# Kernel optimization log

Measured on AMD Instinct MI355X. Metric: run time of the kernel, lower is better.

Reference implementation:

```python
import jax, jax.numpy as jnp
import numpy as np

C = 256          # in_channels == representation_size (GNN(in_channels, in_channels))
REP = 256
H = 300
W = 300
K = 5            # conv/patch kernel
S = 5            # patch stride
KNN = 7          # node_connectivities[0]
HEADS = 8
NH, NW = H // S, W // S
N = NH * NW      # 3600 graph nodes


def setup_inputs() -> dict:
    key = jax.random.key(0)
    ctr = [0]
    def nk():
        ctr[0] += 1
        return jax.random.fold_in(key, ctr[0])
    def rn(shape, s):
        return jax.random.normal(nk(), shape, dtype=jnp.float32) * s
    d = {}
    d['x'] = jax.random.normal(nk(), (1, C, H, W), dtype=jnp.float32)
    d['conv1_w'] = rn((C, C, K, K), 0.02)
    d['conv1_b'] = jnp.zeros((C,), jnp.float32)
    d['fc2_w'] = rn((C, REP), 0.02)
    d['fc2_b'] = jnp.zeros((REP,), jnp.float32)
    d['fc3_w'] = rn((2 * REP, REP), 0.02)
    d['fc3_b'] = jnp.zeros((REP,), jnp.float32)
    def gat(pfx, fin, heads):
        d[pfx + '_wl'] = rn((fin, heads * REP), 0.03)
        d[pfx + '_bl'] = jnp.zeros((heads * REP,), jnp.float32)
        d[pfx + '_wr'] = rn((fin, heads * REP), 0.03)
        d[pfx + '_br'] = jnp.zeros((heads * REP,), jnp.float32)
        d[pfx + '_att'] = rn((heads, REP), 0.1)
        d[pfx + '_bias'] = jnp.zeros((heads * REP,), jnp.float32)
    gat('g1', REP, HEADS)
    gat('g2', HEADS * REP, 1)
    gat('g3', REP, HEADS)
    gat('g4', HEADS * REP, 1)
    return d


def _gatv2(x, wl, bl, wr, br, att, bias, src, dst, mask):
    # PyG GATv2Conv (eval mode, add_self_loops handled by caller via src/dst/mask)
    heads, F = att.shape
    n = x.shape[0]
    xl = (x @ wl + bl).reshape(n, heads, F)   # source transform
    xr = (x @ wr + br).reshape(n, heads, F)   # target transform
    e = jax.nn.leaky_relu(xl[src] + xr[dst], 0.2)          # [E,H,F]
    logit = jnp.einsum('ehf,hf->eh', e, att)               # [E,H]
    logit = jnp.where(mask[:, None], logit, -1e30)
    m = jax.ops.segment_max(logit, dst, num_segments=n)    # every node has a self loop
    ex = jnp.exp(logit - m[dst]) * mask[:, None]
    denom = jax.ops.segment_sum(ex, dst, num_segments=n)
    alpha = ex / denom[dst]
    out = jax.ops.segment_sum(alpha[:, :, None] * xl[src], dst, num_segments=n)
    return out.reshape(n, heads * F) + bias


def _edges_from_topk(vals, idx, strict):
    # torch: A.scatter(1, idx, vals); triu; nonzero -> (row<=col, val!=0);
    # GATv2Conv then removes self loops and adds one per node.
    rows = jnp.arange(N)
    if strict:
        keep = (rows[:, None] < idx) & (vals != 0)
    else:
        keep = (rows[:, None] <= idx) & (vals != 0)  # diag excluded by vals==0 (cdist self-dist)
    src = jnp.concatenate([idx.ravel(), rows])       # source = column index
    dst = jnp.concatenate([jnp.repeat(rows, KNN), rows])  # target = row index
    mask = jnp.concatenate([keep.ravel(), jnp.ones((N,), bool)])
    return src, dst, mask


def _forward(x, conv1_w, conv1_b, fc2_w, fc2_b, fc3_w, fc3_b,
             g1_wl, g1_bl, g1_wr, g1_br, g1_att, g1_bias,
             g2_wl, g2_bl, g2_wr, g2_br, g2_att, g2_bias,
             g3_wl, g3_bl, g3_wr, g3_br, g3_att, g3_bias,
             g4_wl, g4_bl, g4_wr, g4_br, g4_att, g4_bias):
    # --- non-overlapping 5x5 patch embed: unfold + conv(5)->1x1 output ---
    patches = x[0].reshape(C, NH, K, NW, K).transpose(1, 3, 0, 2, 4).reshape(N, C, K, K)
    emb = jax.nn.relu(jnp.einsum('nckl,ockl->no', patches, conv1_w) + conv1_b)
    emb = jax.nn.relu(emb @ fc2_w + fc2_b)  # [N, REP]  (fc1 is unused in the original forward)

    # --- feature-similarity graph: emb @ emb.T, row-wise top-k, triu ---
    adj = emb @ emb.T
    vals, idx = jax.lax.top_k(adj, KNN)
    src1, dst1, m1 = _edges_from_topk(vals, idx, strict=True)

    # --- spatial kNN graph over region centers (cdist, smallest-k, triu) ---
    yy, xx = jnp.meshgrid(jnp.arange(0, H, S, dtype=jnp.float32),
                          jnp.arange(0, W, S, dtype=jnp.float32), indexing='ij')
    centers = jnp.stack([yy.ravel(), xx.ravel()], -1)    # [N,2], i-major like patches
    sq = jnp.sum(centers * centers, -1)
    dist = jnp.sqrt(jnp.maximum(sq[:, None] + sq[None, :] - 2.0 * (centers @ centers.T), 0.0))
    nv, nidx = jax.lax.top_k(-dist, KNN)
    src2, dst2, m2 = _edges_from_topk(-nv, nidx, strict=False)

    h = jax.nn.elu(_gatv2(emb, g1_wl, g1_bl, g1_wr, g1_br, g1_att, g1_bias, src1, dst1, m1))
    h = jax.nn.elu(_gatv2(h, g2_wl, g2_bl, g2_wr, g2_br, g2_att, g2_bias, src1, dst1, m1))
    h_ = jax.nn.elu(_gatv2(emb, g3_wl, g3_bl, g3_wr, g3_br, g3_att, g3_bias, src2, dst2, m2))
    h_ = jax.nn.elu(_gatv2(h_, g4_wl, g4_bl, g4_wr, g4_br, g4_att, g4_bias, src2, dst2, m2))

    hc = jax.nn.relu(jnp.concatenate([h, h_], axis=1) @ fc3_w + fc3_b)
    return hc + h_


def reference(x, conv1_w, conv1_b, fc2_w, fc2_b, fc3_w, fc3_b,
              g1_wl, g1_bl, g1_wr, g1_br, g1_att, g1_bias,
              g2_wl, g2_bl, g2_wr, g2_br, g2_att, g2_bias,
              g3_wl, g3_bl, g3_wr, g3_br, g3_att, g3_bias,
              g4_wl, g4_bl, g4_wr, g4_br, g4_att, g4_bias):
    return _forward(x, conv1_w, conv1_b, fc2_w, fc2_b, fc3_w, fc3_b,
                    g1_wl, g1_bl, g1_wr, g1_br, g1_att, g1_bias,
                    g2_wl, g2_bl, g2_wr, g2_br, g2_att, g2_bias,
                    g3_wl, g3_bl, g3_wr, g3_br, g3_att, g3_bias,
                    g4_wl, g4_bl, g4_wr, g4_br, g4_att, g4_bias)
```

## Files before the change

### kernel.cpp

```cpp
#include <hip/hip_runtime.h>
#include <hip/hip_bf16.h>
#include <math.h>

#define NN 3600
#define HIMG 300
#define WIMG 300
#define NHP 60
#define NCT 57

typedef __attribute__((ext_vector_type(8))) short bf16x8;
typedef __attribute__((ext_vector_type(4))) float f32x4;

__device__ __forceinline__ float bf2f(unsigned short u) {
  union { unsigned int i; float f; } v; v.i = ((unsigned int)u) << 16; return v.f;
}
__device__ __forceinline__ float ldE(const void* p, long i, int md) {
  return md ? bf2f(((const unsigned short*)p)[i]) : ((const float*)p)[i];
}
__device__ __forceinline__ unsigned short f2bf(float f) {
  __hip_bfloat16 h = __float2bfloat16(f);
  return *(unsigned short*)&h;
}

__global__ __launch_bounds__(256) void detect_mode(
    const unsigned short* __restrict__ x, int* __restrict__ flag) {
  __shared__ int bad;
  if (threadIdx.x == 0) bad = 0;
  __syncthreads();
  int b = 0;
  for (int i = threadIdx.x; i < 8192; i += 256) {
    int e = (x[i] >> 7) & 0xFF;
    if (e >= 0x90) b = 1;
  }
  if (b) atomicOr(&bad, 1);
  __syncthreads();
  if (threadIdx.x == 0) {
    flag[0] = bad ? 0 : 1;
    flag[1] = 0;
  }
}

__global__ __launch_bounds__(256) void wtrans(
    const void* __restrict__ w, float* __restrict__ wT, const int* __restrict__ mode) {
  const int md = *mode;
  __shared__ float t[32][33];
  const int k0 = blockIdx.x * 32, o0 = blockIdx.y * 32;
  const int tx = threadIdx.x & 31, ty = threadIdx.x >> 5;
#pragma unroll
  for (int s = 0; s < 32; s += 8)
    t[ty + s][tx] = ldE(w, (long)(o0 + ty + s) * 6400 + k0 + tx, md);
  __syncthreads();
#pragma unroll
  for (int s = 0; s < 32; s += 8)
    wT[(size_t)(k0 + ty + s) * 256 + o0 + tx] = t[tx][ty + s];
}

__global__ __launch_bounds__(256) void wconvT(
    const void* __restrict__ src, unsigned short* __restrict__ dst,
    int Kd, int Nd, const int* __restrict__ mode) {
  const int md = *mode;
  __shared__ float t[32][33];
  const int k0 = blockIdx.x * 32, n0 = blockIdx.y * 32;
  const int tx = threadIdx.x & 31, ty = threadIdx.x >> 5;
#pragma unroll
  for (int s = 0; s < 32; s += 8)
    t[ty + s][tx] = ldE(src, (long)(k0 + ty + s) * Nd + n0 + tx, md);
  __syncthreads();
#pragma unroll
  for (int s = 0; s < 32; s += 8)
    dst[(size_t)(n0 + ty + s) * Kd + k0 + tx] = f2bf(t[tx][ty + s]);
}

__global__ __launch_bounds__(256) void cvt_bf16(
    const float* __restrict__ src, unsigned short* __restrict__ dst, long n4) {
  for (long i = (long)blockIdx.x * 256 + threadIdx.x; i < n4; i += (long)gridDim.x * 256) {
    float4 v = *(const float4*)(src + i * 4);
    ushort4 o;
    o.x = f2bf(v.x); o.y = f2bf(v.y); o.z = f2bf(v.z); o.w = f2bf(v.w);
    *(ushort4*)(dst + i * 4) = o;
  }
}

__global__ __launch_bounds__(256) void im2col(
    const void* __restrict__ x, float* __restrict__ a2, int h, const int* __restrict__ mode) {
  const int md = *mode;
  const int total = NN * 3200;
  for (int i = blockIdx.x * 256 + threadIdx.x; i < total; i += gridDim.x * 256) {
    int n = i / 3200, kl = i - n * 3200;
    int k = h * 3200 + kl;
    int c = k / 25, q = k - c * 25;
    int ki = q / 5, li = q - ki * 5;
    int ni = n / NHP, nj = n - ni * NHP;
    a2[i] = ldE(x, (long)c * (HIMG * WIMG) + (5 * ni + ki) * WIMG + 5 * nj + li, md);
  }
}

__global__ __launch_bounds__(256) void gemm_f84(
    const float* __restrict__ A, const float* __restrict__ B, long boff,
    float* __restrict__ part, int M, int lda, int kchunk, int ldb) {
  __shared__ float As[16][136];
  __shared__ float Bs[16][68];
  const int m0 = blockIdx.y * 128, n0 = blockIdx.x * 64;
  const int z = blockIdx.z;
  const int tid = threadIdx.x;
  const int tr = tid >> 4, tc = tid & 15;
  const int ar = tid >> 1, akq = tid & 1;
  const int bkr = tid >> 4, bnc = tid & 15;
  const int arow = m0 + ar;
  float acc[8][4] = {};

  const int kb = z * kchunk, ke = kb + kchunk;
  for (int k0 = kb; k0 < ke; k0 += 16) {
    __syncthreads();
    {
      float4 v0 = make_float4(0.f, 0.f, 0.f, 0.f), v1 = v0;
      if (arow < M) {
        const float* ap = A + (size_t)arow * lda + k0 + akq * 8;
        v0 = *(const float4*)ap;
        v1 = *(const float4*)(ap + 4);
      }
      As[akq * 8 + 0][ar] = v0.x;
      As[akq * 8 + 1][ar] = v0.y;
      As[akq * 8 + 2][ar] = v0.z;
      As[akq * 8 + 3][ar] = v0.w;
      As[akq * 8 + 4][ar] = v1.x;
      As[akq * 8 + 5][ar] = v1.y;
      As[akq * 8 + 6][ar] = v1.z;
      As[akq * 8 + 7][ar] = v1.w;
    }
    {
      float4 v = *(const float4*)(B + (size_t)(k0 + bkr) * ldb + boff + n0 + bnc * 4);
      Bs[bkr][bnc * 4 + 0] = v.x;
      Bs[bkr][bnc * 4 + 1] = v.y;
      Bs[bkr][bnc * 4 + 2] = v.z;
      Bs[bkr][bnc * 4 + 3] = v.w;
    }
    __syncthreads();
#pragma unroll
    for (int kk = 0; kk < 16; ++kk) {
      float4 a0 = *(const float4*)&As[kk][tr * 8];
      float4 a1 = *(const float4*)&As[kk][tr * 8 + 4];
      float4 bv = *(const float4*)&Bs[kk][tc * 4];
      float a[8] = {a0.x, a0.y, a0.z, a0.w, a1.x, a1.y, a1.z, a1.w};
      float b[4] = {bv.x, bv.y, bv.z, bv.w};
#pragma unroll
      for (int i = 0; i < 8; ++i)
#pragma unroll
        for (int j = 0; j < 4; ++j) acc[i][j] = fmaf(a[i], b[j], acc[i][j]);
    }
  }
#pragma unroll
  for (int i = 0; i < 8; ++i) {
    int row = m0 + tr * 8 + i;
    if (row < M) {
#pragma unroll
      for (int j = 0; j < 4; ++j)
        part[((size_t)z * M + row) * 256 + n0 + tc * 4 + j] = acc[i][j];
    }
  }
}

template <int STORE, int ACT>
__global__ __launch_bounds__(256) void gemm_u(
    const float* __restrict__ A, const void* __restrict__ B0, const void* __restrict__ B1,
    long boff, const void* __restrict__ bias0, const void* __restrict__ bias1, long biasoff,
    float* __restrict__ C0, float* __restrict__ C1, float* __restrict__ part, int cld,
    int M, int lda, int kchunk, int KS, int ldb, const int* __restrict__ mode) {
  const int md = *mode;
  const int z = blockIdx.z;
  const int pair = z / KS, ks = z - pair * KS;
  const void* B = pair ? B1 : B0;
  const void* bias = pair ? bias1 : bias0;
  float* C = pair ? C1 : C0;
  __shared__ float As[16][68];
  __shared__ float Bs[16][68];
  const int m0 = blockIdx.y * 64, n0 = blockIdx.x * 64;
  const int tid = threadIdx.x;
  const int tr = tid >> 4, tc = tid & 15;
  const int ar = tid >> 2, akq = tid & 3;
  const int bkr = tid >> 4, bnc = tid & 15;
  const int arow = m0 + ar;
  float acc[4][4] = {};

  const int kb = ks * kchunk, ke = kb + kchunk;
  for (int k0 = kb; k0 < ke; k0 += 16) {
    __syncthreads();
    {
      float4 v = make_float4(0.f, 0.f, 0.f, 0.f);
      if (arow < M) v = *(const float4*)(A + (size_t)arow * lda + k0 + akq * 4);
      As[akq * 4 + 0][ar] = v.x;
      As[akq * 4 + 1][ar] = v.y;
      As[akq * 4 + 2][ar] = v.z;
      As[akq * 4 + 3][ar] = v.w;
    }
    {
      long bidx = (long)(k0 + bkr) * ldb + boff + n0 + bnc * 4;
      if (md) {
        ushort4 u = *(const ushort4*)((const unsigned short*)B + bidx);
        Bs[bkr][bnc * 4 + 0] = bf2f(u.x);
        Bs[bkr][bnc * 4 + 1] = bf2f(u.y);
        Bs[bkr][bnc * 4 + 2] = bf2f(u.z);
        Bs[bkr][bnc * 4 + 3] = bf2f(u.w);
      } else {
        float4 v = *(const float4*)((const float*)B + bidx);
        Bs[bkr][bnc * 4 + 0] = v.x;
        Bs[bkr][bnc * 4 + 1] = v.y;
        Bs[bkr][bnc * 4 + 2] = v.z;
        Bs[bkr][bnc * 4 + 3] = v.w;
      }
    }
    __syncthreads();
#pragma unroll
    for (int kk = 0; kk < 16; ++kk) {
      float4 av = *(const float4*)&As[kk][tr * 4];
      float4 bv = *(const float4*)&Bs[kk][tc * 4];
      float a[4] = {av.x, av.y, av.z, av.w};
      float b[4] = {bv.x, bv.y, bv.z, bv.w};
#pragma unroll
      for (int i = 0; i < 4; ++i)
#pragma unroll
        for (int j = 0; j < 4; ++j) acc[i][j] = fmaf(a[i], b[j], acc[i][j]);
    }
  }
#pragma unroll
  for (int i = 0; i < 4; ++i) {
    int row = m0 + tr * 4 + i;
    if (row < M) {
#pragma unroll
      for (int j = 0; j < 4; ++j) {
        int col = n0 + tc * 4 + j;
        if (STORE == 2) {
          part[((size_t)z * M + row) * cld + col] = acc[i][j];
        } else if (STORE == 1) {
          C[(size_t)row * cld + col] += acc[i][j];
        } else {
          float v = acc[i][j] + ldE(bias, biasoff + col, md);
          if (ACT == 1) v = fmaxf(v, 0.f);
          C[(size_t)row * cld + col] = v;
        }
      }
    }
  }
}

template <int STORE>
__global__ __launch_bounds__(256) void gemm_mf(
    const unsigned short* __restrict__ A,
    const unsigned short* __restrict__ B0, const unsigned short* __restrict__ B1,
    const void* __restrict__ bias0, const void* __restrict__ bias1,
    float* __restrict__ C0, float* __restrict__ C1, float* __restrict__ part, int cld,
    int M, int K, int kchunk, int KS, const int* __restrict__ mode) {
  const int md = *mode;
  const int z = blockIdx.z;
  const int pair = z / KS, ks = z - pair * KS;
  const unsigned short* B = pair ? B1 : B0;
  const void* bias = pair ? bias1 : bias0;
  float* C = pair ? C1 : C0;

  __shared__ __align__(16) unsigned short Al[128][40];
  __shared__ __align__(16) unsigned short Bl[128][40];
  const int m0 = blockIdx.y * 128, n0 = blockIdx.x * 128;
  const int tid = threadIdx.x;
  const int lane = tid & 63, w = tid >> 6;
  const int wr = (w >> 1) * 64, wc = (w & 1) * 64;
  const int frow = lane & 15, fk = (lane >> 4) * 8;

  f32x4 acc[4][4];
#pragma unroll
  for (int i = 0; i < 4; ++i)
#pragma unroll
    for (int j = 0; j < 4; ++j) acc[i][j] = (f32x4){0.f, 0.f, 0.f, 0.f};

  const int kb0 = ks * kchunk, ke = kb0 + kchunk;
  for (int kb = kb0; kb < ke; kb += 32) {
    __syncthreads();
    for (int c = tid; c < 512; c += 256) {
      int row = c >> 2, kc = (c & 3) << 3;
      uint4 v = make_uint4(0, 0, 0, 0);
      int gr = m0 + row;
      if (gr < M) v = *(const uint4*)(A + (size_t)gr * K + kb + kc);
      *(uint4*)&Al[row][kc] = v;
    }
    for (int c = tid; c < 512; c += 256) {
      int col = c >> 2, kc = (c & 3) << 3;
      uint4 v = *(const uint4*)(B + (size_t)(n0 + col) * K + kb + kc);
      *(uint4*)&Bl[col][kc] = v;
    }
    __syncthreads();

    bf16x8 af[4], bfr[4];
#pragma unroll
    for (int rt = 0; rt < 4; ++rt)
      af[rt] = *(const bf16x8*)&Al[wr + rt * 16 + frow][fk];
#pragma unroll
    for (int ct = 0; ct < 4; ++ct)
      bfr[ct] = *(const bf16x8*)&Bl[wc + ct * 16 + frow][fk];
#pragma unroll
    for (int rt = 0; rt < 4; ++rt)
#pragma unroll
      for (int ct = 0; ct < 4; ++ct)
        acc[rt][ct] = __builtin_amdgcn_mfma_f32_16x16x32_bf16(af[rt], bfr[ct], acc[rt][ct], 0, 0, 0);
  }

#pragma unroll
  for (int rt = 0; rt < 4; ++rt) {
#pragma unroll
    for (int ct = 0; ct < 4; ++ct) {
      int col = n0 + wc + ct * 16 + (lane & 15);
#pragma unroll
      for (int reg = 0; reg < 4; ++reg) {
        int row = m0 + wr + rt * 16 + ((lane >> 4) << 2) + reg;
        if (row < M) {
          float v = acc[rt][ct][reg];
          if (STORE == 2) {
            part[((size_t)z * M + row) * cld + col] = v;
          } else {
            C[(size_t)row * cld + col] = v + ldE(bias, col, md);
          }
        }
      }
    }
  }
}

template <int ACT, int ADDIN, int BIAS>
__global__ __launch_bounds__(256) void reduce_u(
    const float* __restrict__ part, int KS, int M, int ncols,
    const void* __restrict__ bias0, const void* __restrict__ bias1, long biasoff,
    float* __restrict__ C0, float* __restrict__ C1, int cld, const int* __restrict__ mode) {
  const int md = *mode;
  const int pair = blockIdx.z;
  const void* bias = pair ? bias1 : bias0;
  float* C = pair ? C1 : C0;
  size_t total = (size_t)M * ncols;
  for (size_t i = (size_t)blockIdx.x * blockDim.x + threadIdx.x; i < total;
       i += (size_t)gridDim.x * blockDim.x) {
    int row = (int)(i / ncols), col = (int)(i - (size_t)row * ncols);
    float s = ADDIN ? C[(size_t)row * cld + col] : 0.f;
    for (int ks = 0; ks < KS; ++ks)
      s += part[(((size_t)(pair * KS + ks)) * M + row) * ncols + col];
    if (BIAS) s += ldE(bias, biasoff + col, md);
    if (ACT == 1) s = fmaxf(s, 0.f);
    C[(size_t)row * cld + col] = s;
  }
}

__global__ __launch_bounds__(256) void patch_part(
    const void* __restrict__ x, const void* __restrict__ w,
    float* __restrict__ part, int CPB, const int* __restrict__ mode) {
  const int md = *mode;
  __shared__ float As[25][68];
  __shared__ float Bs[25][68];
  const int m0 = blockIdx.y * 64, n0 = blockIdx.x * 64;
  const int tid = threadIdx.x;
  const int tr = tid >> 4, tc = tid & 15;
  const int z = blockIdx.z;
  float acc[4][4] = {};
  const int c0 = z * CPB;
  for (int c = c0; c < c0 + CPB; ++c) {
    __syncthreads();
    for (int e = tid; e < 1600; e += 256) {
      int p = e / 25, q = e - p * 25;
      int ki = q / 5, li = q - ki * 5;
      int n = m0 + p;
      float v = 0.f;
      if (n < NN) {
        int ni = n / NHP, nj = n - ni * NHP;
        v = ldE(x, (long)c * (HIMG * WIMG) + (5 * ni + ki) * WIMG + 5 * nj + li, md);
      }
      As[q][p] = v;
    }
    for (int e = tid; e < 1600; e += 256) {
      int o = e / 25, q = e - o * 25;
      Bs[q][o] = ldE(w, (long)(n0 + o) * 6400 + c * 25 + q, md);
    }
    __syncthreads();
#pragma unroll
    for (int kk = 0; kk < 25; ++kk) {
      float4 av = *(const float4*)&As[kk][tr * 4];
      float4 bv = *(const float4*)&Bs[kk][tc * 4];
      float a[4] = {av.x, av.y, av.z, av.w};
      float b[4] = {bv.x, bv.y, bv.z, bv.w};
#pragma unroll
      for (int i = 0; i < 4; ++i)
#pragma unroll
        for (int j = 0; j < 4; ++j) acc[i][j] = fmaf(a[i], b[j], acc[i][j]);
    }
  }
#pragma unroll
  for (int i = 0; i < 4; ++i) {
    int row = m0 + tr * 4 + i;
    if (row < NN) {
#pragma unroll
      for (int j = 0; j < 4; ++j)
        part[((size_t)z * NN + row) * 256 + n0 + tc * 4 + j] = acc[i][j];
    }
  }
}

__global__ __launch_bounds__(256) void adj_gemm(
    const float* __restrict__ emb, float* __restrict__ pv, unsigned char* __restrict__ pi) {
  __shared__ float As[16][68];
  __shared__ float Bs[16][68];
  __shared__ float mv[64][68];
  __shared__ unsigned char mi[64][68];
  const int m0 = blockIdx.y * 64, n0 = blockIdx.x * 64;
  const int ct = blockIdx.x;
  const int tid = threadIdx.x;
  const int tr = tid >> 4, tc = tid & 15;
  const int ar = tid >> 2, akq = tid & 3;
  const int bn = tid >> 2, bkq = tid & 3;
  const int arow = m0 + ar;
  const int bcol = n0 + bn;
  float acc[4][4] = {};

  for (int k0 = 0; k0 < 256; k0 += 16) {
    __syncthreads();
    {
      float4 v = make_float4(0.f, 0.f, 0.f, 0.f);
      if (arow < NN) v = *(const float4*)(emb + (size_t)arow * 256 + k0 + akq * 4);
      As[akq * 4 + 0][ar] = v.x;
      As[akq * 4 + 1][ar] = v.y;
      As[akq * 4 + 2][ar] = v.z;
      As[akq * 4 + 3][ar] = v.w;
    }
    {
      float4 v = make_float4(0.f, 0.f, 0.f, 0.f);
      if (bcol < NN) v = *(const float4*)(emb + (size_t)bcol * 256 + k0 + bkq * 4);
      Bs[bkq * 4 + 0][bn] = v.x;
      Bs[bkq * 4 + 1][bn] = v.y;
      Bs[bkq * 4 + 2][bn] = v.z;
      Bs[bkq * 4 + 3][bn] = v.w;
    }
    __syncthreads();
#pragma unroll
    for (int kk = 0; kk < 16; ++kk) {
      float4 av = *(const float4*)&As[kk][tr * 4];
      float4 bv = *(const float4*)&Bs[kk][tc * 4];
      float a[4] = {av.x, av.y, av.z, av.w};
      float b[4] = {bv.x, bv.y, bv.z, bv.w};
#pragma unroll
      for (int i = 0; i < 4; ++i)
#pragma unroll
        for (int j = 0; j < 4; ++j) acc[i][j] = fmaf(a[i], b[j], acc[i][j]);
    }
  }

#pragma unroll
  for (int i = 0; i < 4; ++i) {
    float v[4]; int id[4];
#pragma unroll
    for (int j = 0; j < 4; ++j) {
      int cl = tc * 4 + j;
      int valid = (n0 + cl) < NN;
      v[j] = valid ? acc[i][j] : -1e38f;
      id[j] = valid ? cl : 255;
    }
#pragma unroll
    for (int a = 1; a < 4; ++a) {
      float va = v[a]; int ia = id[a];
      int b = a;
      while (b > 0 && (va > v[b - 1] || (va == v[b - 1] && ia < id[b - 1]))) {
        v[b] = v[b - 1]; id[b] = id[b - 1]; --b;
      }
      v[b] = va; id[b] = ia;
    }
    int rl = tr * 4 + i;
#pragma unroll
    for (int s = 0; s < 4; ++s) {
      mv[rl][tc * 4 + s] = v[s];
      mi[rl][tc * 4 + s] = (unsigned char)id[s];
    }
  }
  __syncthreads();

  if (tid < 64) {
    int row = m0 + tid;
    if (row < NN) {
      int ptr[16];
#pragma unroll
      for (int g = 0; g < 16; ++g) ptr[g] = 0;
      for (int k = 0; k < 7; ++k) {
        float best = -1e38f; int bid = 0x7fffffff; int bg = 0;
        for (int g = 0; g < 16; ++g) {
          if (ptr[g] < 4) {
            float vv = mv[tid][g * 4 + ptr[g]];
            int ii = mi[tid][g * 4 + ptr[g]];
            if (vv > best || (vv == best && ii < bid)) { best = vv; bid = ii; bg = g; }
          }
        }
        ptr[bg]++;
        pv[(size_t)row * (NCT * 7) + ct * 7 + k] = best;
        pi[(size_t)row * (NCT * 7) + ct * 7 + k] = (unsigned char)bid;
      }
    }
  }
}

__global__ __launch_bounds__(256) void adj_merge57(
    const float* __restrict__ pv, const unsigned char* __restrict__ pi,
    int* __restrict__ idx_o, int* __restrict__ keep_o) {
  __shared__ unsigned char sp[256][NCT + 3];
  const int t = threadIdx.x;
  const int row = blockIdx.x * 256 + t;
  for (int c = 0; c < NCT; ++c) sp[t][c] = 0;
  if (row >= NN) return;
  const size_t base = (size_t)row * (NCT * 7);
  for (int k = 0; k < 7; ++k) {
    float best = -1e38f; int bidx = 0x7fffffff; int bct = 0;
    for (int c = 0; c < NCT; ++c) {
      int p = sp[t][c];
      if (p < 7) {
        float v = pv[base + c * 7 + p];
        int ii = c * 64 + (int)pi[base + c * 7 + p];
        if (v > best || (v == best && ii < bidx)) { best = v; bidx = ii; bct = c; }
      }
    }
    sp[t][bct]++;
    idx_o[row * 7 + k] = bidx;
    keep_o[row * 7 + k] = (bidx > row && best != 0.0f) ? 1 : 0;
  }
}

__global__ __launch_bounds__(256) void spatial_topk(int* __restrict__ idx_o, int* __restrict__ keep_o) {
  int r = blockIdx.x * 256 + threadIdx.x;
  if (r >= NN) return;
  int ri = r / NHP, rj = r - (r / NHP) * NHP;
  int bd[7], bi[7];
#pragma unroll
  for (int k = 0; k < 7; ++k) { bd[k] = 0x7fffffff; bi[k] = 0x7fffffff; }
  int ilo = ri - 2 > 0 ? ri - 2 : 0, ihi = ri + 2 < NHP - 1 ? ri + 2 : NHP - 1;
  int jlo = rj - 2 > 0 ? rj - 2 : 0, jhi = rj + 2 < NHP - 1 ? rj + 2 : NHP - 1;
  for (int i2 = ilo; i2 <= ihi; ++i2) {
    int dy = ri - i2; int dy2 = dy * dy;
    for (int j2 = jlo; j2 <= jhi; ++j2) {
      int dx = rj - j2;
      int d = dy2 + dx * dx;
      int m = i2 * NHP + j2;
      if (d < bd[6]) {
        int pq = 6;
        while (pq > 0 && d < bd[pq - 1]) { bd[pq] = bd[pq - 1]; bi[pq] = bi[pq - 1]; --pq; }
        bd[pq] = d; bi[pq] = m;
      }
    }
  }
#pragma unroll
  for (int k = 0; k < 7; ++k) {
    idx_o[r * 7 + k] = bi[k];
    keep_o[r * 7 + k] = (bi[k] >= r && bd[k] != 0) ? 1 : 0;
  }
}

__global__ __launch_bounds__(256) void gat_agg1(
    const float* __restrict__ xl, const float* __restrict__ xr,
    const void* __restrict__ att, long attoff, const void* __restrict__ gbias, long gboff,
    const int* __restrict__ nbr, const int* __restrict__ keep,
    float* __restrict__ out, const int* __restrict__ mode) {
  const int md = *mode;
  const int r = blockIdx.x;
  const int f = threadIdx.x;
  __shared__ int s_src[8];
  __shared__ int s_mask_s;
  __shared__ float red[4][8];
  if (f < 7) {
    int v = nbr[r * 7 + f];
    s_src[f] = ((unsigned)v < (unsigned)NN) ? v : 0;
  }
  if (f == 7) s_src[7] = r;
  if (f == 0) {
    int mk = 0x80;
    for (int e = 0; e < 7; ++e)
      if (keep[r * 7 + e] != 0) mk |= (1 << e);
    s_mask_s = mk;
  }
  __syncthreads();
  const int mask = s_mask_s;
  const int wid = f >> 6, lane = f & 63;

  float xrv = xr[(size_t)r * 256 + f];
  float attv = ldE(att, attoff + f, md);
  float xlv[8], part[8];
#pragma unroll
  for (int e = 0; e < 8; ++e) {
    xlv[e] = 0.f; part[e] = 0.f;
    if (mask & (1 << e)) {
      float v = xl[(size_t)s_src[e] * 256 + f];
      xlv[e] = v;
      float s = v + xrv;
      s = s > 0.f ? s : 0.2f * s;
      part[e] = s * attv;
    }
  }
#pragma unroll
  for (int e = 0; e < 8; ++e) {
    float v = part[e];
#pragma unroll
    for (int off = 32; off > 0; off >>= 1) v += __shfl_xor(v, off, 64);
    if (lane == 0) red[wid][e] = v;
  }
  __syncthreads();
  float m = -1e38f;
  float logit[8];
#pragma unroll
  for (int e = 0; e < 8; ++e) {
    logit[e] = red[0][e] + red[1][e] + red[2][e] + red[3][e];
    if (mask & (1 << e)) m = fmaxf(m, logit[e]);
  }
  float den = 0.f, al[8];
#pragma unroll
  for (int e = 0; e < 8; ++e) {
    al[e] = (mask & (1 << e)) ? expf(logit[e] - m) : 0.f;
    den += al[e];
  }
  float inv = 1.0f / den;
  float o = 0.f;
#pragma unroll
  for (int e = 0; e < 8; ++e) o = fmaf(al[e], xlv[e], o);
  o = o * inv + ldE(gbias, gboff + f, md);
  o = o > 0.f ? o : expm1f(o);
  out[(size_t)r * 256 + f] = o;
}

__global__ __launch_bounds__(256) void gat_agg8h(
    const float* __restrict__ xl, const float* __restrict__ xr,
    const void* __restrict__ att, const void* __restrict__ gbias,
    const int* __restrict__ nbr, const int* __restrict__ keep,
    float* __restrict__ out, const int* __restrict__ mode) {
  const int md = *mode;
  const int r = blockIdx.x;
  const int h = blockIdx.y;
  const int f = threadIdx.x;
  __shared__ int s_src[8];
  __shared__ int s_mask_s;
  __shared__ float red[4][8];
  if (f < 7) {
    int v = nbr[r * 7 + f];
    s_src[f] = ((unsigned)v < (unsigned)NN) ? v : 0;
  }
  if (f == 7) s_src[7] = r;
  if (f == 0) {
    int mk = 0x80;
    for (int e = 0; e < 7; ++e)
      if (keep[r * 7 + e] != 0) mk |= (1 << e);
    s_mask_s = mk;
  }
  __syncthreads();
  const int mask = s_mask_s;
  const int wid = f >> 6, lane = f & 63;

  float xrv = xr[(size_t)r * 2048 + h * 256 + f];
  float attv = ldE(att, h * 256 + f, md);
  float xlv[8], part[8];
#pragma unroll
  for (int e = 0; e < 8; ++e) {
    xlv[e] = 0.f; part[e] = 0.f;
    if (mask & (1 << e)) {
      float v = xl[(size_t)s_src[e] * 2048 + h * 256 + f];
      xlv[e] = v;
      float s = v + xrv;
      s = s > 0.f ? s : 0.2f * s;
      part[e] = s * attv;
    }
  }
#pragma unroll
  for (int e = 0; e < 8; ++e) {
    float v = part[e];
#pragma unroll
    for (int off = 32; off > 0; off >>= 1) v += __shfl_xor(v, off, 64);
    if (lane == 0) red[wid][e] = v;
  }
  __syncthreads();
  float m = -1e38f;
  float logit[8];
#pragma unroll
  for (int e = 0; e < 8; ++e) {
    logit[e] = red[0][e] + red[1][e] + red[2][e] + red[3][e];
    if (mask & (1 << e)) m = fmaxf(m, logit[e]);
  }
  float den = 0.f, al[8];
#pragma unroll
  for (int e = 0; e < 8; ++e) {
    al[e] = (mask & (1 << e)) ? expf(logit[e] - m) : 0.f;
    den += al[e];
  }
  float inv = 1.0f / den;
  float o = 0.f;
#pragma unroll
  for (int e = 0; e < 8; ++e) o = fmaf(al[e], xlv[e], o);
  o = o * inv + ldE(gbias, h * 256 + f, md);
  o = o > 0.f ? o : expm1f(o);
  out[(size_t)r * 2048 + h * 256 + f] = o;
}

__global__ __launch_bounds__(256) void fc3_final(
    const float* __restrict__ h2, const float* __restrict__ h4,
    const void* __restrict__ B, const void* __restrict__ bias,
    void* __restrict__ outp, const int* __restrict__ mode) {
  const int md = *mode;
  __shared__ float As[16][68];
  __shared__ float Bs[16][68];
  const int m0 = blockIdx.y * 64, n0 = blockIdx.x * 64;
  const int tid = threadIdx.x;
  const int tr = tid >> 4, tc = tid & 15;
  const int ar = tid >> 2, akq = tid & 3;
  const int bkr = tid >> 4, bnc = tid & 15;
  const int arow = m0 + ar;
  float acc[4][4] = {};

  for (int k0 = 0; k0 < 512; k0 += 16) {
    __syncthreads();
    {
      int k = k0 + akq * 4;
      float4 v = make_float4(0.f, 0.f, 0.f, 0.f);
      if (arow < NN) {
        const float* src = (k < 256) ? (h2 + (size_t)arow * 256 + k)
                                     : (h4 + (size_t)arow * 256 + (k - 256));
        v = *(const float4*)src;
      }
      As[akq * 4 + 0][ar] = v.x;
      As[akq * 4 + 1][ar] = v.y;
      As[akq * 4 + 2][ar] = v.z;
      As[akq * 4 + 3][ar] = v.w;
    }
    {
      long bidx = (long)(k0 + bkr) * 256 + n0 + bnc * 4;
      if (md) {
        ushort4 u = *(const ushort4*)((const unsigned short*)B + bidx);
        Bs[bkr][bnc * 4 + 0] = bf2f(u.x);
        Bs[bkr][bnc * 4 + 1] = bf2f(u.y);
        Bs[bkr][bnc * 4 + 2] = bf2f(u.z);
        Bs[bkr][bnc * 4 + 3] = bf2f(u.w);
      } else {
        float4 v = *(const float4*)((const float*)B + bidx);
        Bs[bkr][bnc * 4 + 0] = v.x;
        Bs[bkr][bnc * 4 + 1] = v.y;
        Bs[bkr][bnc * 4 + 2] = v.z;
        Bs[bkr][bnc * 4 + 3] = v.w;
      }
    }
    __syncthreads();
#pragma unroll
    for (int kk = 0; kk < 16; ++kk) {
      float4 av = *(const float4*)&As[kk][tr * 4];
      float4 bv = *(const float4*)&Bs[kk][tc * 4];
      float a[4] = {av.x, av.y, av.z, av.w};
      float b[4] = {bv.x, bv.y, bv.z, bv.w};
#pragma unroll
      for (int i = 0; i < 4; ++i)
#pragma unroll
        for (int j = 0; j < 4; ++j) acc[i][j] = fmaf(a[i], b[j], acc[i][j]);
    }
  }
#pragma unroll
  for (int i = 0; i < 4; ++i) {
    int row = m0 + tr * 4 + i;
    if (row < NN) {
#pragma unroll
      for (int j = 0; j < 4; ++j) {
        int col = n0 + tc * 4 + j;
        float v = fmaxf(acc[i][j] + ldE(bias, col, md), 0.f) + h4[(size_t)row * 256 + col];
        if (md) ((__hip_bfloat16*)outp)[(size_t)row * 256 + col] = __float2bfloat16(v);
        else ((float*)outp)[(size_t)row * 256 + col] = v;
      }
    }
  }
}

extern "C" void kernel_launch(void* const* d_in, const int* in_sizes, int n_in,
                              void* d_out, int out_size, void* d_ws, size_t ws_size,
                              hipStream_t stream) {
  (void)in_sizes; (void)n_in; (void)out_size;
  const void* x    = d_in[0];
  const void* w1   = d_in[1];
  const void* b1   = d_in[2];
  const void* fc2w = d_in[3];
  const void* fc2b = d_in[4];
  const void* fc3w = d_in[5];
  const void* fc3b = d_in[6];
  const void* g_wl[4]   = {d_in[7],  d_in[13], d_in[19], d_in[25]};
  const void* g_bl[4]   = {d_in[8],  d_in[14], d_in[20], d_in[26]};
  const void* g_wr[4]   = {d_in[9],  d_in[15], d_in[21], d_in[27]};
  const void* g_br[4]   = {d_in[10], d_in[16], d_in[22], d_in[28]};
  const void* g_att[4]  = {d_in[11], d_in[17], d_in[23], d_in[29]};
  const void* g_bias[4] = {d_in[12], d_in[18], d_in[24], d_in[30]};

  float* ws = (float*)d_ws;
  int* mode = (int*)d_ws;
  size_t off = 64;
  float* emb = ws + off; off += (size_t)NN * 256;
  float* xl2 = ws + off; off += (size_t)NN * 256;
  float* xr2 = ws + off; off += (size_t)NN * 256;
  float* h2  = ws + off; off += (size_t)NN * 256;
  float* h4  = ws + off; off += (size_t)NN * 256;
  int* idx1  = (int*)(ws + off); off += NN * 7;
  int* keep1 = (int*)(ws + off); off += NN * 7;
  int* idx2  = (int*)(ws + off); off += NN * 7;
  int* keep2 = (int*)(ws + off); off += NN * 7;
  unsigned short* emb_bf = (unsigned short*)(ws + off); off += (size_t)NN * 256 / 2;
  unsigned short* wbfL   = (unsigned short*)(ws + off); off += (size_t)524288 / 2;
  unsigned short* wbfR   = (unsigned short*)(ws + off); off += (size_t)524288 / 2;
  float* scratch = ws + off;
  const size_t wide_need = off + 3 * (size_t)NN * 2048;
  const bool wide = ws_size >= wide_need * sizeof(float);

  float* emb1 = h2;
  float* pv = scratch;
  unsigned char* pi = (unsigned char*)(scratch + (size_t)NN * (NCT * 7));

  dim3 blk(256);
  const int* idxs[2]  = {idx1, idx2};
  const int* keeps[2] = {keep1, keep2};
  float* houts[2] = {h2, h4};
  const int* f32mode = mode + 1;

  detect_mode<<<dim3(1), blk, 0, stream>>>((const unsigned short*)x, mode);

  if (wide) {
    float* wT   = scratch;
    float* part = wT + (size_t)6400 * 256;
    float* a2   = part + 8 * (size_t)NN * 256;

    wtrans<<<dim3(200, 8), blk, 0, stream>>>(w1, wT, mode);
    for (int h = 0; h < 2; ++h) {
      im2col<<<dim3(2048), blk, 0, stream>>>(x, a2, h, mode);
      gemm_f84<<<dim3(4, 29, 8), blk, 0, stream>>>(a2, wT, (long)h * 3200 * 256,
                                                   part, NN, 3200, 400, 256);
      if (h == 0)
        reduce_u<0, 0, 0><<<dim3(1024, 1, 1), blk, 0, stream>>>(part, 8, NN, 256,
                                                                b1, b1, 0, emb1, emb1, 256, mode);
      else
        reduce_u<1, 1, 1><<<dim3(1024, 1, 1), blk, 0, stream>>>(part, 8, NN, 256,
                                                                b1, b1, 0, emb1, emb1, 256, mode);
    }
  } else {
    const int convKS = 2;
    patch_part<<<dim3(4, 57, convKS), blk, 0, stream>>>(x, w1, scratch, 256 / convKS, mode);
    reduce_u<1, 0, 1><<<dim3(1024, 1, 1), blk, 0, stream>>>(scratch, convKS, NN, 256,
                                                            b1, b1, 0, emb1, emb1, 256, mode);
  }

  gemm_u<0, 1><<<dim3(4, 57, 1), blk, 0, stream>>>(emb1, fc2w, fc2w, 0, fc2b, fc2b, 0,
                                                   emb, emb, nullptr, 256,
                                                   NN, 256, 256, 1, 256, mode);
  adj_gemm<<<dim3(NCT, NCT), blk, 0, stream>>>(emb, pv, pi);
  adj_merge57<<<dim3(15), blk, 0, stream>>>(pv, pi, idx1, keep1);
  spatial_topk<<<dim3(15), blk, 0, stream>>>(idx2, keep2);

  if (wide) {
    float* xl_w = scratch;
    float* xr_w = xl_w + (size_t)NN * 2048;
    float* hh_w = xr_w + (size_t)NN * 2048;
    unsigned short* hh_bf = (unsigned short*)xl_w;
    float* g24part = xr_w;

    cvt_bf16<<<dim3(512), blk, 0, stream>>>(emb, emb_bf, (long)NN * 64);

    for (int g = 0; g < 2; ++g) {
      int a = g * 2, b = g * 2 + 1;
      wconvT<<<dim3(8, 64), blk, 0, stream>>>(g_wl[a], wbfL, 256, 2048, mode);
      wconvT<<<dim3(8, 64), blk, 0, stream>>>(g_wr[a], wbfR, 256, 2048, mode);
      gemm_mf<0><<<dim3(16, 29, 2), blk, 0, stream>>>(emb_bf, wbfL, wbfR,
                                                      g_bl[a], g_br[a],
                                                      xl_w, xr_w, nullptr, 2048,
                                                      NN, 256, 256, 1, mode);
      gat_agg8h<<<dim3(NN, 8), blk, 0, stream>>>(xl_w, xr_w, g_att[a], g_bias[a],
                                                 idxs[g], keeps[g], hh_w, mode);
      cvt_bf16<<<dim3(2048), blk, 0, stream>>>(hh_w, hh_bf, (long)NN * 512);
      wconvT<<<dim3(64, 8), blk, 0, stream>>>(g_wl[b], wbfL, 2048, 256, mode);
      wconvT<<<dim3(64, 8), blk, 0, stream>>>(g_wr[b], wbfR, 2048, 256, mode);
      gemm_mf<2><<<dim3(2, 29, 8), blk, 0, stream>>>(hh_bf, wbfL, wbfR,
                                                     nullptr, nullptr,
                                                     nullptr, nullptr, g24part, 256,
                                                     NN, 2048, 512, 4, mode);
      reduce_u<0, 0, 1><<<dim3(1024, 1, 2), blk, 0, stream>>>(g24part, 4, NN, 256,
                                                              g_bl[b], g_br[b], 0,
                                                              xl2, xr2, 256, mode);
      gat_agg1<<<dim3(NN), blk, 0, stream>>>(xl2, xr2, g_att[b], 0, g_bias[b], 0,
                                             idxs[g], keeps[g], houts[g], mode);
    }
  } else {
    float* xlh = scratch;
    float* xrh = xlh + (size_t)NN * 256;
    float* hh  = xrh + (size_t)NN * 256;

    for (int g = 0; g < 2; ++g) {
      int a = g * 2, b = g * 2 + 1;
      for (int h = 0; h < 8; ++h) {
        gemm_u<0, 0><<<dim3(4, 57, 2), blk, 0, stream>>>(emb, g_wl[a], g_wr[a], h * 256,
                                                         g_bl[a], g_br[a], h * 256,
                                                         xlh, xrh, nullptr, 256,
                                                         NN, 256, 256, 1, 2048, mode);
        gat_agg1<<<dim3(NN), blk, 0, stream>>>(xlh, xrh, g_att[a], h * 256, g_bias[a], h * 256,
                                               idxs[g], keeps[g], hh, mode);
        if (h == 0) {
          gemm_u<0, 0><<<dim3(4, 57, 2), blk, 0, stream>>>(hh, g_wl[b], g_wr[b], 0,
                                                           g_bl[b], g_br[b], 0,
                                                           xl2, xr2, nullptr, 256,
                                                           NN, 256, 256, 1, 256, mode);
        } else {
          gemm_u<1, 0><<<dim3(4, 57, 2), blk, 0, stream>>>(hh, g_wl[b], g_wr[b], (long)h * 256 * 256,
                                                           g_bl[b], g_br[b], 0,
                                                           xl2, xr2, nullptr, 256,
                                                           NN, 256, 256, 1, 256, mode);
        }
      }
      gat_agg1<<<dim3(NN), blk, 0, stream>>>(xl2, xr2, g_att[b], 0, g_bias[b], 0,
                                             idxs[g], keeps[g], houts[g], mode);
    }
  }

  fc3_final<<<dim3(4, 57), blk, 0, stream>>>(h2, h4, fc3w, fc3b, d_out, mode);
}
```

Before: 1.077 ms.

## Prefetch GEMM tiles into registers, parallelize top-k merge per wavefront, fuse weight conversions

Three GEMM kernels (gemm_f84, gemm_mf, adj_gemm) now load the next K-tile into registers while the current tile is computed, so global load latency overlaps with math. adj_merge57 changes from one thread per row over 15 blocks to one wavefront per row over 900 blocks, using shuffle-based argmax to merge the 57 partial top-7 lists. The paired wconvT launches are fused into a single wconvT2 launch over a z-dimension. The prefetching adds register pressure and could lower occupancy.

```diff
diff --git a/kernel.cpp b/kernel.cpp
--- a/kernel.cpp
+++ b/kernel.cpp
@@ -55,10 +55,13 @@
     wT[(size_t)(k0 + ty + s) * 256 + o0 + tx] = t[tx][ty + s];
 }
 
-__global__ __launch_bounds__(256) void wconvT(
-    const void* __restrict__ src, unsigned short* __restrict__ dst,
+__global__ __launch_bounds__(256) void wconvT2(
+    const void* __restrict__ srcL, const void* __restrict__ srcR,
+    unsigned short* __restrict__ dstL, unsigned short* __restrict__ dstR,
     int Kd, int Nd, const int* __restrict__ mode) {
   const int md = *mode;
+  const void* src = blockIdx.z ? srcR : srcL;
+  unsigned short* dst = blockIdx.z ? dstR : dstL;
   __shared__ float t[32][33];
   const int k0 = blockIdx.x * 32, n0 = blockIdx.y * 32;
   const int tx = threadIdx.x & 31, ty = threadIdx.x >> 5;
@@ -110,32 +113,37 @@
   float acc[8][4] = {};
 
   const int kb = z * kchunk, ke = kb + kchunk;
+  float4 pa0 = make_float4(0.f, 0.f, 0.f, 0.f), pa1 = pa0, pb;
+  if (arow < M) {
+    const float* ap = A + (size_t)arow * lda + kb + akq * 8;
+    pa0 = *(const float4*)ap;
+    pa1 = *(const float4*)(ap + 4);
+  }
+  pb = *(const float4*)(B + (size_t)(kb + bkr) * ldb + boff + n0 + bnc * 4);
+
   for (int k0 = kb; k0 < ke; k0 += 16) {
     __syncthreads();
-    {
-      float4 v0 = make_float4(0.f, 0.f, 0.f, 0.f), v1 = v0;
+    As[akq * 8 + 0][ar] = pa0.x;
+    As[akq * 8 + 1][ar] = pa0.y;
+    As[akq * 8 + 2][ar] = pa0.z;
+    As[akq * 8 + 3][ar] = pa0.w;
+    As[akq * 8 + 4][ar] = pa1.x;
+    As[akq * 8 + 5][ar] = pa1.y;
+    As[akq * 8 + 6][ar] = pa1.z;
+    As[akq * 8 + 7][ar] = pa1.w;
+    Bs[bkr][bnc * 4 + 0] = pb.x;
+    Bs[bkr][bnc * 4 + 1] = pb.y;
+    Bs[bkr][bnc * 4 + 2] = pb.z;
+    Bs[bkr][bnc * 4 + 3] = pb.w;
+    __syncthreads();
+    if (k0 + 16 < ke) {
       if (arow < M) {
-        const float* ap = A + (size_t)arow * lda + k0 + akq * 8;
-        v0 = *(const float4*)ap;
-        v1 = *(const float4*)(ap + 4);
-      }
-      As[akq * 8 + 0][ar] = v0.x;
-      As[akq * 8 + 1][ar] = v0.y;
-      As[akq * 8 + 2][ar] = v0.z;
-      As[akq * 8 + 3][ar] = v0.w;
-      As[akq * 8 + 4][ar] = v1.x;
-      As[akq * 8 + 5][ar] = v1.y;
-      As[akq * 8 + 6][ar] = v1.z;
-      As[akq * 8 + 7][ar] = v1.w;
-    }
-    {
-      float4 v = *(const float4*)(B + (size_t)(k0 + bkr) * ldb + boff + n0 + bnc * 4);
-      Bs[bkr][bnc * 4 + 0] = v.x;
-      Bs[bkr][bnc * 4 + 1] = v.y;
-      Bs[bkr][bnc * 4 + 2] = v.z;
-      Bs[bkr][bnc * 4 + 3] = v.w;
-    }
-    __syncthreads();
+        const float* ap = A + (size_t)arow * lda + (k0 + 16) + akq * 8;
+        pa0 = *(const float4*)ap;
+        pa1 = *(const float4*)(ap + 4);
+      }
+      pb = *(const float4*)(B + (size_t)(k0 + 16 + bkr) * ldb + boff + n0 + bnc * 4);
+    }
 #pragma unroll
     for (int kk = 0; kk < 16; ++kk) {
       float4 a0 = *(const float4*)&As[kk][tr * 8];
@@ -264,6 +272,8 @@
   const int lane = tid & 63, w = tid >> 6;
   const int wr = (w >> 1) * 64, wc = (w & 1) * 64;
   const int frow = lane & 15, fk = (lane >> 4) * 8;
+  const int sr0 = tid >> 2, skc0 = (tid & 3) << 3;
+  const int sr1 = (tid + 256) >> 2, skc1 = ((tid + 256) & 3) << 3;
 
   f32x4 acc[4][4];
 #pragma unroll
@@ -272,21 +282,31 @@
     for (int j = 0; j < 4; ++j) acc[i][j] = (f32x4){0.f, 0.f, 0.f, 0.f};
 
   const int kb0 = ks * kchunk, ke = kb0 + kchunk;
+  uint4 qa0 = make_uint4(0, 0, 0, 0), qa1 = qa0, qb0, qb1;
+  {
+    int gr0 = m0 + sr0, gr1 = m0 + sr1;
+    if (gr0 < M) qa0 = *(const uint4*)(A + (size_t)gr0 * K + kb0 + skc0);
+    if (gr1 < M) qa1 = *(const uint4*)(A + (size_t)gr1 * K + kb0 + skc1);
+    qb0 = *(const uint4*)(B + (size_t)(n0 + sr0) * K + kb0 + skc0);
+    qb1 = *(const uint4*)(B + (size_t)(n0 + sr1) * K + kb0 + skc1);
+  }
+
   for (int kb = kb0; kb < ke; kb += 32) {
     __syncthreads();
-    for (int c = tid; c < 512; c += 256) {
-      int row = c >> 2, kc = (c & 3) << 3;
-      uint4 v = make_uint4(0, 0, 0, 0);
-      int gr = m0 + row;
-      if (gr < M) v = *(const uint4*)(A + (size_t)gr * K + kb + kc);
-      *(uint4*)&Al[row][kc] = v;
-    }
-    for (int c = tid; c < 512; c += 256) {
-      int col = c >> 2, kc = (c & 3) << 3;
-      uint4 v = *(const uint4*)(B + (size_t)(n0 + col) * K + kb + kc);
-      *(uint4*)&Bl[col][kc] = v;
-    }
-    __syncthreads();
+    *(uint4*)&Al[sr0][skc0] = qa0;
+    *(uint4*)&Al[sr1][skc1] = qa1;
+    *(uint4*)&Bl[sr0][skc0] = qb0;
+    *(uint4*)&Bl[sr1][skc1] = qb1;
+    __syncthreads();
+    if (kb + 32 < ke) {
+      int kn = kb + 32;
+      int gr0 = m0 + sr0, gr1 = m0 + sr1;
+      qa0 = make_uint4(0, 0, 0, 0); qa1 = qa0;
+      if (gr0 < M) qa0 = *(const uint4*)(A + (size_t)gr0 * K + kn + skc0);
+      if (gr1 < M) qa1 = *(const uint4*)(A + (size_t)gr1 * K + kn + skc1);
+      qb0 = *(const uint4*)(B + (size_t)(n0 + sr0) * K + kn + skc0);
+      qb1 = *(const uint4*)(B + (size_t)(n0 + sr1) * K + kn + skc1);
+    }
 
     bf16x8 af[4], bfr[4];
 #pragma unroll
@@ -414,25 +434,25 @@
   const int bcol = n0 + bn;
   float acc[4][4] = {};
 
+  float4 fa = make_float4(0.f, 0.f, 0.f, 0.f), fb = fa;
+  if (arow < NN) fa = *(const float4*)(emb + (size_t)arow * 256 + akq * 4);
+  if (bcol < NN) fb = *(const float4*)(emb + (size_t)bcol * 256 + bkq * 4);
+
   for (int k0 = 0; k0 < 256; k0 += 16) {
     __syncthreads();
-    {
-      float4 v = make_float4(0.f, 0.f, 0.f, 0.f);
-      if (arow < NN) v = *(const float4*)(emb + (size_t)arow * 256 + k0 + akq * 4);
-      As[akq * 4 + 0][ar] = v.x;
-      As[akq * 4 + 1][ar] = v.y;
-      As[akq * 4 + 2][ar] = v.z;
-      As[akq * 4 + 3][ar] = v.w;
-    }
-    {
-      float4 v = make_float4(0.f, 0.f, 0.f, 0.f);
-      if (bcol < NN) v = *(const float4*)(emb + (size_t)bcol * 256 + k0 + bkq * 4);
-      Bs[bkq * 4 + 0][bn] = v.x;
-      Bs[bkq * 4 + 1][bn] = v.y;
-      Bs[bkq * 4 + 2][bn] = v.z;
-      Bs[bkq * 4 + 3][bn] = v.w;
-    }
-    __syncthreads();
+    As[akq * 4 + 0][ar] = fa.x;
+    As[akq * 4 + 1][ar] = fa.y;
+    As[akq * 4 + 2][ar] = fa.z;
+    As[akq * 4 + 3][ar] = fa.w;
+    Bs[bkq * 4 + 0][bn] = fb.x;
+    Bs[bkq * 4 + 1][bn] = fb.y;
+    Bs[bkq * 4 + 2][bn] = fb.z;
+    Bs[bkq * 4 + 3][bn] = fb.w;
+    __syncthreads();
+    if (k0 + 16 < 256) {
+      if (arow < NN) fa = *(const float4*)(emb + (size_t)arow * 256 + k0 + 16 + akq * 4);
+      if (bcol < NN) fb = *(const float4*)(emb + (size_t)bcol * 256 + k0 + 16 + bkq * 4);
+    }
 #pragma unroll
     for (int kk = 0; kk < 16; ++kk) {
       float4 av = *(const float4*)&As[kk][tr * 4];
@@ -500,25 +520,38 @@
 __global__ __launch_bounds__(256) void adj_merge57(
     const float* __restrict__ pv, const unsigned char* __restrict__ pi,
     int* __restrict__ idx_o, int* __restrict__ keep_o) {
-  __shared__ unsigned char sp[256][NCT + 3];
-  const int t = threadIdx.x;
-  const int row = blockIdx.x * 256 + t;
-  for (int c = 0; c < NCT; ++c) sp[t][c] = 0;
+  const int wid = threadIdx.x >> 6, lane = threadIdx.x & 63;
+  const int row = blockIdx.x * 4 + wid;
   if (row >= NN) return;
   const size_t base = (size_t)row * (NCT * 7);
+  int p = 0;
+  float mval = -1e38f;
+  int mid = 0x7fffffff;
+  if (lane < NCT) {
+    mval = pv[base + lane * 7];
+    mid = lane * 64 + (int)pi[base + lane * 7];
+  }
   for (int k = 0; k < 7; ++k) {
-    float best = -1e38f; int bidx = 0x7fffffff; int bct = 0;
-    for (int c = 0; c < NCT; ++c) {
-      int p = sp[t][c];
+    float v = mval; int i = mid;
+#pragma unroll
+    for (int off = 32; off > 0; off >>= 1) {
+      float ov = __shfl_xor(v, off, 64);
+      int oi = __shfl_xor(i, off, 64);
+      if (ov > v || (ov == v && oi < i)) { v = ov; i = oi; }
+    }
+    if (lane == 0) {
+      idx_o[row * 7 + k] = i;
+      keep_o[row * 7 + k] = (i > row && v != 0.0f) ? 1 : 0;
+    }
+    if (mval == v && mid == i) {
+      ++p;
       if (p < 7) {
-        float v = pv[base + c * 7 + p];
-        int ii = c * 64 + (int)pi[base + c * 7 + p];
-        if (v > best || (v == best && ii < bidx)) { best = v; bidx = ii; bct = c; }
-      }
-    }
-    sp[t][bct]++;
-    idx_o[row * 7 + k] = bidx;
-    keep_o[row * 7 + k] = (bidx > row && best != 0.0f) ? 1 : 0;
+        mval = pv[base + lane * 7 + p];
+        mid = lane * 64 + (int)pi[base + lane * 7 + p];
+      } else {
+        mval = -1e38f; mid = 0x7fffffff;
+      }
+    }
   }
 }
 
@@ -843,7 +876,7 @@
                                                    emb, emb, nullptr, 256,
                                                    NN, 256, 256, 1, 256, mode);
   adj_gemm<<<dim3(NCT, NCT), blk, 0, stream>>>(emb, pv, pi);
-  adj_merge57<<<dim3(15), blk, 0, stream>>>(pv, pi, idx1, keep1);
+  adj_merge57<<<dim3(900), blk, 0, stream>>>(pv, pi, idx1, keep1);
   spatial_topk<<<dim3(15), blk, 0, stream>>>(idx2, keep2);
 
   if (wide) {
@@ -857,8 +890,7 @@
 
     for (int g = 0; g < 2; ++g) {
       int a = g * 2, b = g * 2 + 1;
-      wconvT<<<dim3(8, 64), blk, 0, stream>>>(g_wl[a], wbfL, 256, 2048, mode);
-      wconvT<<<dim3(8, 64), blk, 0, stream>>>(g_wr[a], wbfR, 256, 2048, mode);
+      wconvT2<<<dim3(8, 64, 2), blk, 0, stream>>>(g_wl[a], g_wr[a], wbfL, wbfR, 256, 2048, mode);
       gemm_mf<0><<<dim3(16, 29, 2), blk, 0, stream>>>(emb_bf, wbfL, wbfR,
                                                       g_bl[a], g_br[a],
                                                       xl_w, xr_w, nullptr, 2048,
@@ -866,8 +898,7 @@
       gat_agg8h<<<dim3(NN, 8), blk, 0, stream>>>(xl_w, xr_w, g_att[a], g_bias[a],
                                                  idxs[g], keeps[g], hh_w, mode);
       cvt_bf16<<<dim3(2048), blk, 0, stream>>>(hh_w, hh_bf, (long)NN * 512);
-      wconvT<<<dim3(64, 8), blk, 0, stream>>>(g_wl[b], wbfL, 2048, 256, mode);
-      wconvT<<<dim3(64, 8), blk, 0, stream>>>(g_wr[b], wbfR, 2048, 256, mode);
+      wconvT2<<<dim3(64, 8, 2), blk, 0, stream>>>(g_wl[b], g_wr[b], wbfL, wbfR, 2048, 256, mode);
       gemm_mf<2><<<dim3(2, 29, 8), blk, 0, stream>>>(hh_bf, wbfL, wbfR,
                                                      nullptr, nullptr,
                                                      nullptr, nullptr, g24part, 256,
```

Result: faster. 920.4 us (-14.5%).
